# Optimization experiments

Hardware: AMD Instinct MI355X
Metric: run time of the kernel (lower is better)

Reference implementation:

```python
import jax, jax.numpy as jnp
import numpy as np

B, L, DM = 2, 1024, 768
DI = 2 * DM            # d_inner = 1536
NS = 16                # d_state
DTR = 48               # dt_rank
SCALE = 15             # scale_bits


def _dsp(x):
    # DampenedSquareplus: 0.5 * squareplus(x) = 0.25*(x + sqrt(x^2+4))
    return 0.25 * (x + jnp.sqrt(x * x + 4.0))


def _forward(hidden_states, gamma, W_in, b_in, conv_w, conv_b, W_x, b_x,
             W_dt, b_dt, W_out, b_out, base_decay_nums, res_gate, decay_shifts):
    residual = hidden_states
    # BitShiftNorm: center, then power-of-two RMS scale
    xm = hidden_states - hidden_states.mean(axis=-1, keepdims=True)
    var = (xm * xm).mean(axis=-1, keepdims=True)
    k = jnp.maximum(jnp.round(jnp.log2(jnp.sqrt(var + 1e-9))), 0.0)
    hs = xm * (2.0 ** (-k)) * gamma
    # in_proj (BitLinear modeled as linear)
    xz = hs @ W_in.T + b_in                      # [B,L,2*DI]
    x, z = jnp.split(xz, 2, axis=-1)             # each [B,L,DI]
    # causal depthwise conv1d (kernel 4, left pad 3, truncate to L)
    xt = jnp.transpose(x, (0, 2, 1))             # [B,DI,L]
    xt = jax.lax.conv_general_dilated(
        xt, conv_w, window_strides=(1,), padding=[(3, 0)],
        dimension_numbers=('NCH', 'OIH', 'NCH'), feature_group_count=DI)
    xt = xt + conv_b[None, :, None]
    x = jnp.transpose(xt, (0, 2, 1))             # [B,L,DI]
    x = _dsp(x)
    # x_proj -> dt, B_ssm, C_ssm
    x_dbl = x @ W_x.T + b_x                      # [B,L,DTR+2*NS]
    dt = x_dbl[..., :DTR]
    B_ssm = x_dbl[..., DTR:DTR + NS]
    C_ssm = x_dbl[..., DTR + NS:]
    decay_mod = dt @ W_dt.T + b_dt               # [B,L,DI]
    decay_nums = jnp.clip(base_decay_nums[None, None] + decay_mod[..., None], 0.0, 32767.0)  # [B,L,DI,NS]
    dt_val = _dsp(decay_mod) * 0.1               # [B,L,DI]
    u = (x * dt_val)[..., None] * B_ssm[:, :, None, :]   # [B,L,DI,NS]
    # dyadic decay: a = nums * 2^{-shift}
    a = decay_nums * (2.0 ** (-decay_shifts.astype(jnp.float32)))[None, None]
    F = DI * NS
    u_f = u.reshape(B, L, F)
    a_f = a.reshape(B, L, F)
    # linear recurrence h_t = a_t*h_{t-1} + u_t via associative scan over L
    def combine(c1, c2):
        a1, b1 = c1
        a2, b2 = c2
        return (a1 * a2, a2 * b1 + b2)
    _, h_f = jax.lax.associative_scan(combine, (a_f, u_f), axis=1)
    h_f = jnp.clip(h_f, -32000.0, 32000.0)
    h = h_f.reshape(B, L, DI, NS)
    y = jnp.einsum('bldn,bln->bld', h, C_ssm)    # [B,L,DI]
    # RationalSigmoid gate
    gate = 0.5 * (1.0 + z / jnp.sqrt(z * z + 1.0))
    y = y * gate
    out = y @ W_out.T + b_out
    out = jnp.clip(out, -32000.0, 32000.0)
    return residual + out * res_gate


def setup_inputs() -> dict:
    key = jax.random.key(0)
    ks = jax.random.split(key, 8)
    hidden_states = jax.random.normal(ks[0], (B, L, DM), jnp.float32)
    gamma = jnp.ones((DM,), jnp.float32)
    W_in = jax.random.normal(ks[1], (2 * DI, DM), jnp.float32) / np.float32(np.sqrt(DM))
    b_in = jnp.zeros((2 * DI,), jnp.float32)
    conv_w = jax.random.normal(ks[2], (DI, 1, 4), jnp.float32) * 0.5
    conv_b = jnp.zeros((DI,), jnp.float32)
    W_x = jax.random.normal(ks[3], (DTR + 2 * NS, DI), jnp.float32) / np.float32(np.sqrt(DI))
    b_x = jnp.zeros((DTR + 2 * NS,), jnp.float32)
    W_dt = jax.random.normal(ks[4], (DI, DTR), jnp.float32) * 0.001
    b_dt = jnp.zeros((DI,), jnp.float32)
    W_out = jax.random.normal(ks[5], (DM, DI), jnp.float32) * np.float32(0.02 / np.sqrt(24))
    b_out = jnp.zeros((DM,), jnp.float32)
    # HiPPO-S4D-real-like decays projected to dyadic with shift=15
    n = jnp.arange(NS, dtype=jnp.float32)
    decays = jnp.exp(-0.01 * (n + 1.0))
    base = jnp.round(decays * (2.0 ** SCALE))
    base_decay_nums = jnp.tile(base[None, :], (DI, 1))
    decay_shifts = jnp.full((DI, NS), SCALE, jnp.int32)
    res_gate = jnp.full((1,), 0.5, jnp.float32)  # nonzero so output depends on branch
    return dict(hidden_states=hidden_states, gamma=gamma, W_in=W_in, b_in=b_in,
                conv_w=conv_w, conv_b=conv_b, W_x=W_x, b_x=b_x, W_dt=W_dt, b_dt=b_dt,
                W_out=W_out, b_out=b_out, base_decay_nums=base_decay_nums,
                res_gate=res_gate, decay_shifts=decay_shifts)


def reference(hidden_states, gamma, W_in, b_in, conv_w, conv_b, W_x, b_x,
              W_dt, b_dt, W_out, b_out, base_decay_nums, res_gate, decay_shifts):
    return _forward(hidden_states, gamma, W_in, b_in, conv_w, conv_b, W_x, b_x,
                    W_dt, b_dt, W_out, b_out, base_decay_nums, res_gate, decay_shifts)
```

## Files before the change

kernel.cpp:

```cpp
#include <hip/hip_runtime.h>
#include <hip/hip_bf16.h>
#include <stdint.h>

#define BB  2
#define LL  1024
#define DMM 768
#define DII 1536
#define NSS 16
#define DTRR 48
#define XZN (2*DII)
#define NROWS (BB*LL)
#define N2 1664

#define CHUNKS 64
#define CHLEN  (LL/CHUNKS)
#define NCH    (BB*DII*NSS)

typedef _Float16 h16;
typedef __attribute__((ext_vector_type(8))) _Float16 h16x8;
typedef __attribute__((ext_vector_type(4))) float f32x4;

typedef const __attribute__((address_space(1))) uint32_t gau32;
typedef __attribute__((address_space(3))) uint32_t lau32;
#define GLL16(gp, lp) __builtin_amdgcn_global_load_lds((gau32*)(gp), (lau32*)(lp), 16, 0, 0)

__device__ __forceinline__ float dspf(float x) {
    return 0.25f * (x + sqrtf(x*x + 4.0f));
}
__device__ __forceinline__ float clampf(float x, float lo, float hi) {
    return fminf(fmaxf(x, lo), hi);
}

__global__ __launch_bounds__(256) void k_cvt(const float* __restrict__ in,
                                             h16* __restrict__ out, int n) {
    int i = blockIdx.x * 256 + threadIdx.x;
    if (i < n) out[i] = (h16)in[i];
}

__global__ __launch_bounds__(256) void k_w2(const float* __restrict__ W_x,
                                            const float* __restrict__ b_x,
                                            const float* __restrict__ W_dt,
                                            const float* __restrict__ b_dt,
                                            h16* __restrict__ W2,
                                            float* __restrict__ bias2) {
    int i = blockIdx.x;
    int tid = threadIdx.x;
    if (i < DII) {
        __shared__ float wd[DTRR];
        if (tid < DTRR) wd[tid] = W_dt[i * DTRR + tid];
        __syncthreads();
        for (int j = tid; j < DII; j += 256) {
            float s = 0.f;
            #pragma unroll
            for (int k = 0; k < DTRR; ++k) s = fmaf(wd[k], W_x[(size_t)k * DII + j], s);
            W2[(size_t)i * DII + j] = (h16)s;
        }
        if (tid == 0) {
            float s = b_dt[i];
            for (int k = 0; k < DTRR; ++k) s = fmaf(wd[k], b_x[k], s);
            bias2[i] = s;
        }
    } else if (i < DII + 2 * NSS) {
        int r = i - DII;
        for (int j = tid; j < DII; j += 256)
            W2[(size_t)i * DII + j] = (h16)W_x[(size_t)(DTRR + r) * DII + j];
        if (tid == 0) bias2[i] = b_x[DTRR + r];
    } else {
        for (int j = tid; j < DII; j += 256) W2[(size_t)i * DII + j] = (h16)0.f;
        if (tid == 0) bias2[i] = 0.f;
    }
}

__global__ __launch_bounds__(256) void k_norm(const float* __restrict__ hs,
                                              const float* __restrict__ gamma,
                                              h16* __restrict__ out) {
    int row = blockIdx.x;
    const float* p = hs + (size_t)row * DMM;
    __shared__ float red[256];
    int tid = threadIdx.x;

    float s = 0.f;
    for (int i = tid; i < DMM; i += 256) s += p[i];
    red[tid] = s; __syncthreads();
    for (int off = 128; off > 0; off >>= 1) {
        if (tid < off) red[tid] += red[tid + off];
        __syncthreads();
    }
    float mean = red[0] / (float)DMM;
    __syncthreads();

    float v = 0.f;
    for (int i = tid; i < DMM; i += 256) { float d = p[i] - mean; v += d*d; }
    red[tid] = v; __syncthreads();
    for (int off = 128; off > 0; off >>= 1) {
        if (tid < off) red[tid] += red[tid + off];
        __syncthreads();
    }
    float var = red[0] / (float)DMM;
    float k = rintf(log2f(sqrtf(var + 1e-9f)));
    k = fmaxf(k, 0.f);
    float scale = exp2f(-k);
    for (int i = tid; i < DMM; i += 256)
        out[(size_t)row * DMM + i] = (h16)((p[i] - mean) * scale * gamma[i]);
}

template<int EPI, typename OutT>
__global__ __launch_bounds__(256) void k_gemm64(
    const h16* __restrict__ A, int lda,
    const h16* __restrict__ Bw, int ldb,
    const float* __restrict__ bias,
    OutT* __restrict__ C, int ldc, int K,
    const float* __restrict__ resid, const float* __restrict__ rgate)
{
    __shared__ __align__(16) h16 As[2][64 * 64];
    __shared__ __align__(16) h16 Bs[2][64 * 64];
    const int tid  = threadIdx.x;
    const int lane = tid & 63;
    const int wv   = tid >> 6;

    const int nwg = gridDim.x * gridDim.y;
    const int bid = blockIdx.y * gridDim.x + blockIdx.x;
    const int cpx = nwg >> 3;
    const int swz = (bid & 7) * cpx + (bid >> 3);
    const int bxi = swz % gridDim.x, byi = swz / gridDim.x;

    const int bm = byi * 64, bn = bxi * 64;
    const int wr = wv >> 1, wc = wv & 1;

    f32x4 acc[2][2] = {};

    const int srow = lane >> 3;
    const int kbl  = ((lane & 7) ^ srow) * 8;
    const int KT = K / 64;

    #pragma unroll
    for (int q = 0; q < 2; ++q) {
        int row = (wv * 2 + q) * 8 + srow;
        GLL16(A  + (size_t)(bm + row) * lda + kbl, &As[0][(wv*2+q)*8*64]);
        GLL16(Bw + (size_t)(bn + row) * ldb + kbl, &Bs[0][(wv*2+q)*8*64]);
    }

    int buf = 0;
    for (int kt = 0; kt < KT; ++kt) {
        if (kt + 1 < KT) {
            int k0 = (kt + 1) * 64;
            #pragma unroll
            for (int q = 0; q < 2; ++q) {
                int row = (wv * 2 + q) * 8 + srow;
                GLL16(A  + (size_t)(bm + row) * lda + k0 + kbl, &As[buf^1][(wv*2+q)*8*64]);
                GLL16(Bw + (size_t)(bn + row) * ldb + k0 + kbl, &Bs[buf^1][(wv*2+q)*8*64]);
            }
            asm volatile("s_waitcnt vmcnt(4)" ::: "memory");
        } else {
            asm volatile("s_waitcnt vmcnt(0)" ::: "memory");
        }
        __syncthreads();

        const int r16 = lane & 15, kq = lane >> 4;
        #pragma unroll
        for (int kk = 0; kk < 2; ++kk) {
            h16x8 af[2], bf[2];
            #pragma unroll
            for (int i = 0; i < 2; ++i) {
                int rowA = wr * 32 + i * 16 + r16;
                af[i] = *(const h16x8*)&As[buf][rowA * 64 + (((kk*4 + kq) ^ (rowA & 7)) << 3)];
            }
            #pragma unroll
            for (int j = 0; j < 2; ++j) {
                int rowB = wc * 32 + j * 16 + r16;
                bf[j] = *(const h16x8*)&Bs[buf][rowB * 64 + (((kk*4 + kq) ^ (rowB & 7)) << 3)];
            }
            #pragma unroll
            for (int i = 0; i < 2; ++i)
                #pragma unroll
                for (int j = 0; j < 2; ++j)
                    acc[i][j] = __builtin_amdgcn_mfma_f32_16x16x32_f16(af[i], bf[j], acc[i][j], 0, 0, 0);
        }
        __syncthreads();
        buf ^= 1;
    }

    const int r4 = (lane >> 4) * 4;
    const int cn = lane & 15;
    float rg = 0.f;
    if (EPI) rg = rgate[0];
    #pragma unroll
    for (int i = 0; i < 2; ++i) {
        #pragma unroll
        for (int j = 0; j < 2; ++j) {
            int col = bn + wc * 32 + j * 16 + cn;
            float bv = bias[col];
            #pragma unroll
            for (int r = 0; r < 4; ++r) {
                int row = bm + wr * 32 + i * 16 + r4 + r;
                float v = acc[i][j][r] + bv;
                if (EPI) {
                    v = clampf(v, -32000.f, 32000.f);
                    v = resid[(size_t)row * ldc + col] + v * rg;
                }
                C[(size_t)row * ldc + col] = (OutT)v;
            }
        }
    }
}

__global__ __launch_bounds__(256) void k_conv(const h16* __restrict__ xz,
                                              const float* __restrict__ cw,
                                              const float* __restrict__ cb,
                                              h16* __restrict__ xacth)
{
    int idx = blockIdx.x * 256 + threadIdx.x;
    if (idx >= NROWS * DII) return;
    int c = idx % DII;
    int bl = idx / DII;
    int l = bl % LL;
    int b = bl / LL;
    float acc = cb[c];
    #pragma unroll
    for (int j = 0; j < 4; ++j) {
        int ls = l - 3 + j;
        if (ls >= 0)
            acc = fmaf((float)xz[(size_t)(b * LL + ls) * XZN + c], cw[c * 4 + j], acc);
    }
    xacth[idx] = (h16)dspf(acc);
}

__device__ __forceinline__ void load_setup(const float* __restrict__ basenum,
                                           const int* __restrict__ shifts,
                                           int d, float* base, float* p2c) {
    const float4* bp = (const float4*)(basenum + (size_t)d * NSS);
    const int4*   sp = (const int4*)(shifts + (size_t)d * NSS);
    #pragma unroll
    for (int q = 0; q < 4; ++q) {
        float4 bv = bp[q]; int4 sv = sp[q];
        base[q*4+0] = bv.x; base[q*4+1] = bv.y; base[q*4+2] = bv.z; base[q*4+3] = bv.w;
        p2c[q*4+0] = exp2f(-(float)sv.x);
        p2c[q*4+1] = exp2f(-(float)sv.y);
        p2c[q*4+2] = exp2f(-(float)sv.z);
        p2c[q*4+3] = exp2f(-(float)sv.w);
    }
}

__global__ __launch_bounds__(256) void k_scan_p1(
    const h16* __restrict__ dmbc,
    const h16* __restrict__ xacth,
    const float* __restrict__ basenum,
    const int*   __restrict__ shifts,
    float* __restrict__ stA, float* __restrict__ stH)
{
    int bc   = blockIdx.x / 6;
    int dblk = blockIdx.x % 6;
    int d    = dblk * 256 + threadIdx.x;
    int b    = bc / CHUNKS;
    int chunk= bc % CHUNKS;

    float base[16], p2c[16], h[16], A[16];
    load_setup(basenum, shifts, d, base, p2c);
    #pragma unroll
    for (int n = 0; n < 16; ++n) { h[n] = 0.f; A[n] = 1.f; }

    int row0 = b * LL + chunk * CHLEN;
    #pragma unroll 4
    for (int l = 0; l < CHLEN; ++l) {
        int row = row0 + l;
        float dm = (float)dmbc[(size_t)row * N2 + d];
        float xv = (float)xacth[(size_t)row * DII + d];
        float common = xv * (dspf(dm) * 0.1f);
        const h16x8* Bp = (const h16x8*)(dmbc + (size_t)row * N2 + DII);
        h16x8 b0 = Bp[0], b1 = Bp[1];
        float Bv[16];
        #pragma unroll
        for (int n = 0; n < 8; ++n) { Bv[n] = (float)b0[n]; Bv[8+n] = (float)b1[n]; }
        #pragma unroll
        for (int n = 0; n < 16; ++n) {
            float a = clampf(base[n] + dm, 0.f, 32767.f) * p2c[n];
            h[n] = fmaf(a, h[n], common * Bv[n]);
            A[n] *= a;
        }
    }
    size_t sb = ((size_t)bc * DII + d) * 16;
    float4* pa = (float4*)(stA + sb);
    float4* ph = (float4*)(stH + sb);
    #pragma unroll
    for (int q = 0; q < 4; ++q) {
        pa[q] = make_float4(A[q*4+0], A[q*4+1], A[q*4+2], A[q*4+3]);
        ph[q] = make_float4(h[q*4+0], h[q*4+1], h[q*4+2], h[q*4+3]);
    }
}

__global__ __launch_bounds__(256) void k_scan_p2(float* __restrict__ stA,
                                                 const float* __restrict__ stH)
{
    int ch = blockIdx.x * 256 + threadIdx.x;
    int b  = ch / (DII * NSS);
    int rem = ch - b * (DII * NSS);
    float hin = 0.f;
    #pragma unroll 4
    for (int c = 0; c < CHUNKS; ++c) {
        size_t idx = ((size_t)(b * CHUNKS + c) * (DII * NSS)) + rem;
        float a = stA[idx], hh = stH[idx];
        stA[idx] = hin;
        hin = fmaf(a, hin, hh);
    }
}

__global__ __launch_bounds__(256) void k_scan_p3(
    const h16* __restrict__ dmbc,
    const h16* __restrict__ xacth,
    const h16* __restrict__ xz,
    const float* __restrict__ basenum,
    const int*   __restrict__ shifts,
    const float* __restrict__ stA,
    h16* __restrict__ ygh)
{
    int bc   = blockIdx.x / 6;
    int dblk = blockIdx.x % 6;
    int d    = dblk * 256 + threadIdx.x;
    int b    = bc / CHUNKS;
    int chunk= bc % CHUNKS;

    float base[16], p2c[16], h[16];
    load_setup(basenum, shifts, d, base, p2c);
    size_t sb = ((size_t)bc * DII + d) * 16;
    const float4* pa = (const float4*)(stA + sb);
    #pragma unroll
    for (int q = 0; q < 4; ++q) {
        float4 v = pa[q];
        h[q*4+0] = v.x; h[q*4+1] = v.y; h[q*4+2] = v.z; h[q*4+3] = v.w;
    }

    int row0 = b * LL + chunk * CHLEN;
    #pragma unroll 4
    for (int l = 0; l < CHLEN; ++l) {
        int row = row0 + l;
        float dm = (float)dmbc[(size_t)row * N2 + d];
        float xv = (float)xacth[(size_t)row * DII + d];
        float common = xv * (dspf(dm) * 0.1f);
        const h16x8* Bp = (const h16x8*)(dmbc + (size_t)row * N2 + DII);
        h16x8 b0 = Bp[0], b1 = Bp[1], c0 = Bp[2], c1 = Bp[3];
        float Bv[16], Cv[16];
        #pragma unroll
        for (int n = 0; n < 8; ++n) {
            Bv[n] = (float)b0[n]; Bv[8+n] = (float)b1[n];
            Cv[n] = (float)c0[n]; Cv[8+n] = (float)c1[n];
        }
        float y = 0.f;
        #pragma unroll
        for (int n = 0; n < 16; ++n) {
            float a = clampf(base[n] + dm, 0.f, 32767.f) * p2c[n];
            h[n] = fmaf(a, h[n], common * Bv[n]);
            float hc = clampf(h[n], -32000.f, 32000.f);
            y = fmaf(hc, Cv[n], y);
        }
        float z = (float)xz[(size_t)row * XZN + DII + d];
        float gate = 0.5f * (1.0f + z * rsqrtf(z * z + 1.0f));
        ygh[(size_t)row * DII + d] = (h16)(y * gate);
    }
}

extern "C" void kernel_launch(void* const* d_in, const int* in_sizes, int n_in,
                              void* d_out, int out_size, void* d_ws, size_t ws_size,
                              hipStream_t stream) {
    const float* hs        = (const float*)d_in[0];
    const float* gamma     = (const float*)d_in[1];
    const float* W_in      = (const float*)d_in[2];
    const float* b_in      = (const float*)d_in[3];
    const float* conv_w    = (const float*)d_in[4];
    const float* conv_b    = (const float*)d_in[5];
    const float* W_x       = (const float*)d_in[6];
    const float* b_x       = (const float*)d_in[7];
    const float* W_dt      = (const float*)d_in[8];
    const float* b_dt      = (const float*)d_in[9];
    const float* W_out     = (const float*)d_in[10];
    const float* b_out     = (const float*)d_in[11];
    const float* base_dec  = (const float*)d_in[12];
    const float* res_gate  = (const float*)d_in[13];
    const int*   dec_shift = (const int*)d_in[14];

    char* w = (char*)d_ws;
    h16*   XZH   = (h16*)w;    w += (size_t)NROWS * XZN * 2;
    h16*   XACTH = (h16*)w;    w += (size_t)NROWS * DII * 2;
    h16*   DMBCH = (h16*)w;    w += (size_t)NROWS * N2  * 2;
    h16*   W2H   = (h16*)w;    w += (size_t)N2 * DII * 2;
    h16*   WOH   = (h16*)w;    w += (size_t)DMM * DII * 2;
    float* BIAS2 = (float*)w;  w += 8192;
    h16*   YGH   = (h16*)w;    w += (size_t)NROWS * DII * 2;
    h16*   HSNH  = (h16*)w;    w += (size_t)NROWS * DMM * 2;
    h16*   WINH  = (h16*)w;    w += (size_t)XZN * DMM * 2;
    float* STA   = (float*)w;  w += (size_t)BB * CHUNKS * DII * NSS * 4;
    float* STH   = (float*)w;  w += (size_t)BB * CHUNKS * DII * NSS * 4;

    float* out = (float*)d_out;

    k_cvt<<<(XZN * DMM + 255) / 256, 256, 0, stream>>>(W_in, WINH, XZN * DMM);
    k_cvt<<<(DMM * DII + 255) / 256, 256, 0, stream>>>(W_out, WOH, DMM * DII);
    k_w2<<<N2, 256, 0, stream>>>(W_x, b_x, W_dt, b_dt, W2H, BIAS2);

    k_norm<<<NROWS, 256, 0, stream>>>(hs, gamma, HSNH);

    k_gemm64<0, h16><<<dim3(XZN / 64, NROWS / 64), 256, 0, stream>>>(
        HSNH, DMM, WINH, DMM, b_in, XZH, XZN, DMM, nullptr, nullptr);

    k_conv<<<(NROWS * DII) / 256, 256, 0, stream>>>(XZH, conv_w, conv_b, XACTH);

    k_gemm64<0, h16><<<dim3(N2 / 64, NROWS / 64), 256, 0, stream>>>(
        XACTH, DII, W2H, DII, BIAS2, DMBCH, N2, DII, nullptr, nullptr);

    k_scan_p1<<<BB * CHUNKS * 6, 256, 0, stream>>>(
        DMBCH, XACTH, base_dec, dec_shift, STA, STH);
    k_scan_p2<<<NCH / 256, 256, 0, stream>>>(STA, STH);
    k_scan_p3<<<BB * CHUNKS * 6, 256, 0, stream>>>(
        DMBCH, XACTH, XZH, base_dec, dec_shift, STA, YGH);

    k_gemm64<1, float><<<dim3(DMM / 64, NROWS / 64), 256, 0, stream>>>(
        YGH, DII, WOH, DII, b_out, out, DMM, DII, hs, res_gate);
}
```

Baseline: 176.6 us.

## Load GEMM B-operand directly to registers and vectorize norm, conv, conversion kernels

The GEMM now stages only A through LDS and loads B fragments straight from global memory into registers with a manually unrolled two-stage ping-pong, and its tile-index swizzle is changed to column-major block order. The z-gate activation moves into the in_proj GEMM epilogue, removing that work from the scan kernel. Norm uses one wave per row with float4 loads and shuffle reductions, conv processes 8 channels per thread with vector loads, and the two weight-conversion kernels merge into one launch. The direct B loads skip LDS reuse across waves, so B traffic rises and the load latency may be exposed.

After: 239.7 us. 1.36x slower.

```diff
diff --git a/kernel.cpp b/kernel.cpp
--- a/kernel.cpp
+++ b/kernel.cpp
@@ -31,10 +31,13 @@
     return fminf(fmaxf(x, lo), hi);
 }
 
-__global__ __launch_bounds__(256) void k_cvt(const float* __restrict__ in,
-                                             h16* __restrict__ out, int n) {
+__global__ __launch_bounds__(256) void k_cvt2(const float* __restrict__ in1,
+                                              h16* __restrict__ out1, int n1,
+                                              const float* __restrict__ in2,
+                                              h16* __restrict__ out2, int n2) {
     int i = blockIdx.x * 256 + threadIdx.x;
-    if (i < n) out[i] = (h16)in[i];
+    if (i < n1) out1[i] = (h16)in1[i];
+    else if (i < n1 + n2) out2[i - n1] = (h16)in2[i - n1];
 }
 
 __global__ __launch_bounds__(256) void k_w2(const float* __restrict__ W_x,
@@ -74,38 +77,43 @@
 __global__ __launch_bounds__(256) void k_norm(const float* __restrict__ hs,
                                               const float* __restrict__ gamma,
                                               h16* __restrict__ out) {
-    int row = blockIdx.x;
+    int row  = blockIdx.x * 4 + (threadIdx.x >> 6);
+    int lane = threadIdx.x & 63;
     const float* p = hs + (size_t)row * DMM;
-    __shared__ float red[256];
-    int tid = threadIdx.x;
-
-    float s = 0.f;
-    for (int i = tid; i < DMM; i += 256) s += p[i];
-    red[tid] = s; __syncthreads();
-    for (int off = 128; off > 0; off >>= 1) {
-        if (tid < off) red[tid] += red[tid + off];
-        __syncthreads();
-    }
-    float mean = red[0] / (float)DMM;
-    __syncthreads();
-
-    float v = 0.f;
-    for (int i = tid; i < DMM; i += 256) { float d = p[i] - mean; v += d*d; }
-    red[tid] = v; __syncthreads();
-    for (int off = 128; off > 0; off >>= 1) {
-        if (tid < off) red[tid] += red[tid + off];
-        __syncthreads();
-    }
-    float var = red[0] / (float)DMM;
+    float4 v0 = *(const float4*)&p[lane * 4];
+    float4 v1 = *(const float4*)&p[256 + lane * 4];
+    float4 v2 = *(const float4*)&p[512 + lane * 4];
+    float s = v0.x+v0.y+v0.z+v0.w + v1.x+v1.y+v1.z+v1.w + v2.x+v2.y+v2.z+v2.w;
+    #pragma unroll
+    for (int off = 32; off > 0; off >>= 1) s += __shfl_xor(s, off);
+    float mean = s * (1.0f / (float)DMM);
+    float vv = 0.f;
+    #pragma unroll
+    for (int q = 0; q < 4; ++q) {
+        float d0 = ((const float*)&v0)[q] - mean; vv += d0*d0;
+        float d1 = ((const float*)&v1)[q] - mean; vv += d1*d1;
+        float d2 = ((const float*)&v2)[q] - mean; vv += d2*d2;
+    }
+    #pragma unroll
+    for (int off = 32; off > 0; off >>= 1) vv += __shfl_xor(vv, off);
+    float var = vv * (1.0f / (float)DMM);
     float k = rintf(log2f(sqrtf(var + 1e-9f)));
     k = fmaxf(k, 0.f);
     float scale = exp2f(-k);
-    for (int i = tid; i < DMM; i += 256)
-        out[(size_t)row * DMM + i] = (h16)((p[i] - mean) * scale * gamma[i]);
+    float4 g0 = *(const float4*)&gamma[lane * 4];
+    float4 g1 = *(const float4*)&gamma[256 + lane * 4];
+    float4 g2 = *(const float4*)&gamma[512 + lane * 4];
+    h16* o = out + (size_t)row * DMM;
+    #pragma unroll
+    for (int q = 0; q < 4; ++q) {
+        o[lane*4 + q]       = (h16)((((const float*)&v0)[q] - mean) * scale * ((const float*)&g0)[q]);
+        o[256 + lane*4 + q] = (h16)((((const float*)&v1)[q] - mean) * scale * ((const float*)&g1)[q]);
+        o[512 + lane*4 + q] = (h16)((((const float*)&v2)[q] - mean) * scale * ((const float*)&g2)[q]);
+    }
 }
 
 template<int EPI, typename OutT>
-__global__ __launch_bounds__(256) void k_gemm64(
+__global__ __launch_bounds__(256) void k_gemm_bd(
     const h16* __restrict__ A, int lda,
     const h16* __restrict__ Bw, int ldb,
     const float* __restrict__ bias,
@@ -113,17 +121,16 @@
     const float* __restrict__ resid, const float* __restrict__ rgate)
 {
     __shared__ __align__(16) h16 As[2][64 * 64];
-    __shared__ __align__(16) h16 Bs[2][64 * 64];
     const int tid  = threadIdx.x;
     const int lane = tid & 63;
     const int wv   = tid >> 6;
 
-    const int nwg = gridDim.x * gridDim.y;
-    const int bid = blockIdx.y * gridDim.x + blockIdx.x;
+    const int gy = gridDim.y;
+    const int nwg = gridDim.x * gy;
+    const int bid0 = blockIdx.x * gy + blockIdx.y;
     const int cpx = nwg >> 3;
-    const int swz = (bid & 7) * cpx + (bid >> 3);
-    const int bxi = swz % gridDim.x, byi = swz / gridDim.x;
-
+    const int swz = (bid0 & 7) * cpx + (bid0 >> 3);
+    const int bxi = swz / gy, byi = swz % gy;
     const int bm = byi * 64, bn = bxi * 64;
     const int wr = wv >> 1, wc = wv & 1;
 
@@ -133,57 +140,71 @@
     const int kbl  = ((lane & 7) ^ srow) * 8;
     const int KT = K / 64;
 
-    #pragma unroll
-    for (int q = 0; q < 2; ++q) {
-        int row = (wv * 2 + q) * 8 + srow;
-        GLL16(A  + (size_t)(bm + row) * lda + kbl, &As[0][(wv*2+q)*8*64]);
-        GLL16(Bw + (size_t)(bn + row) * ldb + kbl, &Bs[0][(wv*2+q)*8*64]);
-    }
-
-    int buf = 0;
-    for (int kt = 0; kt < KT; ++kt) {
-        if (kt + 1 < KT) {
-            int k0 = (kt + 1) * 64;
-            #pragma unroll
-            for (int q = 0; q < 2; ++q) {
-                int row = (wv * 2 + q) * 8 + srow;
-                GLL16(A  + (size_t)(bm + row) * lda + k0 + kbl, &As[buf^1][(wv*2+q)*8*64]);
-                GLL16(Bw + (size_t)(bn + row) * ldb + k0 + kbl, &Bs[buf^1][(wv*2+q)*8*64]);
-            }
-            asm volatile("s_waitcnt vmcnt(4)" ::: "memory");
+    const int r16 = lane & 15, kq = lane >> 4;
+    const size_t bofs0 = (size_t)(bn + wc * 32 + r16) * ldb + (kq << 3);
+    const size_t bofs1 = bofs0 + (size_t)16 * ldb;
+
+    h16x8 bfA[2][2], bfB[2][2];
+
+#define STAGEA(dstbuf, k0) do { \
+    _Pragma("unroll") \
+    for (int q = 0; q < 2; ++q) { \
+        int row_ = (wv * 2 + q) * 8 + srow; \
+        GLL16(A + (size_t)(bm + row_) * lda + (k0) + kbl, &As[dstbuf][(wv*2+q)*8*64]); \
+    } } while (0)
+
+#define LOADB(BF, k0) do { \
+    BF[0][0] = *(const h16x8*)&Bw[bofs0 + (k0)]; \
+    BF[0][1] = *(const h16x8*)&Bw[bofs1 + (k0)]; \
+    BF[1][0] = *(const h16x8*)&Bw[bofs0 + (k0) + 32]; \
+    BF[1][1] = *(const h16x8*)&Bw[bofs1 + (k0) + 32]; \
+    } while (0)
+
+#define COMPUTE(abuf, BF) do { \
+    _Pragma("unroll") \
+    for (int kk = 0; kk < 2; ++kk) { \
+        int rowA0 = wr * 32 + r16, rowA1 = rowA0 + 16; \
+        h16x8 af0 = *(const h16x8*)&As[abuf][rowA0 * 64 + (((kk*4 + kq) ^ (rowA0 & 7)) << 3)]; \
+        h16x8 af1 = *(const h16x8*)&As[abuf][rowA1 * 64 + (((kk*4 + kq) ^ (rowA1 & 7)) << 3)]; \
+        acc[0][0] = __builtin_amdgcn_mfma_f32_16x16x32_f16(af0, BF[kk][0], acc[0][0], 0, 0, 0); \
+        acc[0][1] = __builtin_amdgcn_mfma_f32_16x16x32_f16(af0, BF[kk][1], acc[0][1], 0, 0, 0); \
+        acc[1][0] = __builtin_amdgcn_mfma_f32_16x16x32_f16(af1, BF[kk][0], acc[1][0], 0, 0, 0); \
+        acc[1][1] = __builtin_amdgcn_mfma_f32_16x16x32_f16(af1, BF[kk][1], acc[1][1], 0, 0, 0); \
+    } } while (0)
+
+    STAGEA(0, 0);
+    LOADB(bfA, 0);
+
+    for (int ktp = 0; ktp < KT; ktp += 2) {
+        if (ktp + 1 < KT) {
+            STAGEA(1, (ktp + 1) * 64);
+            LOADB(bfB, (ktp + 1) * 64);
+            asm volatile("s_waitcnt vmcnt(6)" ::: "memory");
         } else {
             asm volatile("s_waitcnt vmcnt(0)" ::: "memory");
         }
         __syncthreads();
-
-        const int r16 = lane & 15, kq = lane >> 4;
-        #pragma unroll
-        for (int kk = 0; kk < 2; ++kk) {
-            h16x8 af[2], bf[2];
-            #pragma unroll
-            for (int i = 0; i < 2; ++i) {
-                int rowA = wr * 32 + i * 16 + r16;
-                af[i] = *(const h16x8*)&As[buf][rowA * 64 + (((kk*4 + kq) ^ (rowA & 7)) << 3)];
-            }
-            #pragma unroll
-            for (int j = 0; j < 2; ++j) {
-                int rowB = wc * 32 + j * 16 + r16;
-                bf[j] = *(const h16x8*)&Bs[buf][rowB * 64 + (((kk*4 + kq) ^ (rowB & 7)) << 3)];
-            }
-            #pragma unroll
-            for (int i = 0; i < 2; ++i)
-                #pragma unroll
-                for (int j = 0; j < 2; ++j)
-                    acc[i][j] = __builtin_amdgcn_mfma_f32_16x16x32_f16(af[i], bf[j], acc[i][j], 0, 0, 0);
-        }
+        COMPUTE(0, bfA);
         __syncthreads();
-        buf ^= 1;
-    }
+        if (ktp + 2 < KT) {
+            STAGEA(0, (ktp + 2) * 64);
+            LOADB(bfA, (ktp + 2) * 64);
+            asm volatile("s_waitcnt vmcnt(6)" ::: "memory");
+        } else {
+            asm volatile("s_waitcnt vmcnt(0)" ::: "memory");
+        }
+        __syncthreads();
+        COMPUTE(1, bfB);
+        __syncthreads();
+    }
+#undef STAGEA
+#undef LOADB
+#undef COMPUTE
 
     const int r4 = (lane >> 4) * 4;
     const int cn = lane & 15;
     float rg = 0.f;
-    if (EPI) rg = rgate[0];
+    if (EPI == 1) rg = rgate[0];
     #pragma unroll
     for (int i = 0; i < 2; ++i) {
         #pragma unroll
@@ -194,9 +215,12 @@
             for (int r = 0; r < 4; ++r) {
                 int row = bm + wr * 32 + i * 16 + r4 + r;
                 float v = acc[i][j][r] + bv;
-                if (EPI) {
+                if (EPI == 1) {
                     v = clampf(v, -32000.f, 32000.f);
                     v = resid[(size_t)row * ldc + col] + v * rg;
+                }
+                if (EPI == 2) {
+                    if (col >= DII) v = 0.5f * (1.0f + v * rsqrtf(v * v + 1.0f));
                 }
                 C[(size_t)row * ldc + col] = (OutT)v;
             }
@@ -210,19 +234,34 @@
                                               h16* __restrict__ xacth)
 {
     int idx = blockIdx.x * 256 + threadIdx.x;
-    if (idx >= NROWS * DII) return;
-    int c = idx % DII;
-    int bl = idx / DII;
+    if (idx >= NROWS * (DII / 8)) return;
+    int c8 = idx % (DII / 8);
+    int bl = idx / (DII / 8);
     int l = bl % LL;
     int b = bl / LL;
-    float acc = cb[c];
-    #pragma unroll
-    for (int j = 0; j < 4; ++j) {
-        int ls = l - 3 + j;
-        if (ls >= 0)
-            acc = fmaf((float)xz[(size_t)(b * LL + ls) * XZN + c], cw[c * 4 + j], acc);
-    }
-    xacth[idx] = (h16)dspf(acc);
+    int c0 = c8 * 8;
+
+    float acc[8];
+    float4 wv[8];
+    #pragma unroll
+    for (int j = 0; j < 8; ++j) {
+        acc[j] = cb[c0 + j];
+        wv[j] = *(const float4*)&cw[(c0 + j) * 4];
+    }
+    #pragma unroll
+    for (int t = 0; t < 4; ++t) {
+        int ls = l - 3 + t;
+        if (ls >= 0) {
+            h16x8 xv = *(const h16x8*)&xz[(size_t)(b * LL + ls) * XZN + c0];
+            #pragma unroll
+            for (int j = 0; j < 8; ++j)
+                acc[j] = fmaf((float)xv[j], ((const float*)&wv[j])[t], acc[j]);
+        }
+    }
+    h16x8 o;
+    #pragma unroll
+    for (int j = 0; j < 8; ++j) o[j] = (h16)dspf(acc[j]);
+    *(h16x8*)&xacth[(size_t)bl * DII + c0] = o;
 }
 
 __device__ __forceinline__ void load_setup(const float* __restrict__ basenum,
@@ -352,8 +391,7 @@
             float hc = clampf(h[n], -32000.f, 32000.f);
             y = fmaf(hc, Cv[n], y);
         }
-        float z = (float)xz[(size_t)row * XZN + DII + d];
-        float gate = 0.5f * (1.0f + z * rsqrtf(z * z + 1.0f));
+        float gate = (float)xz[(size_t)row * XZN + DII + d];
         ygh[(size_t)row * DII + d] = (h16)(y * gate);
     }
 }
@@ -392,18 +430,18 @@
 
     float* out = (float*)d_out;
 
-    k_cvt<<<(XZN * DMM + 255) / 256, 256, 0, stream>>>(W_in, WINH, XZN * DMM);
-    k_cvt<<<(DMM * DII + 255) / 256, 256, 0, stream>>>(W_out, WOH, DMM * DII);
+    k_cvt2<<<(XZN * DMM + DMM * DII + 255) / 256, 256, 0, stream>>>(
+        W_in, WINH, XZN * DMM, W_out, WOH, DMM * DII);
     k_w2<<<N2, 256, 0, stream>>>(W_x, b_x, W_dt, b_dt, W2H, BIAS2);
 
-    k_norm<<<NROWS, 256, 0, stream>>>(hs, gamma, HSNH);
-
-    k_gemm64<0, h16><<<dim3(XZN / 64, NROWS / 64), 256, 0, stream>>>(
+    k_norm<<<NROWS / 4, 256, 0, stream>>>(hs, gamma, HSNH);
+
+    k_gemm_bd<2, h16><<<dim3(XZN / 64, NROWS / 64), 256, 0, stream>>>(
         HSNH, DMM, WINH, DMM, b_in, XZH, XZN, DMM, nullptr, nullptr);
 
-    k_conv<<<(NROWS * DII) / 256, 256, 0, stream>>>(XZH, conv_w, conv_b, XACTH);
-
-    k_gemm64<0, h16><<<dim3(N2 / 64, NROWS / 64), 256, 0, stream>>>(
+    k_conv<<<(NROWS * (DII / 8)) / 256, 256, 0, stream>>>(XZH, conv_w, conv_b, XACTH);
+
+    k_gemm_bd<0, h16><<<dim3(N2 / 64, NROWS / 64), 256, 0, stream>>>(
         XACTH, DII, W2H, DII, BIAS2, DMBCH, N2, DII, nullptr, nullptr);
 
     k_scan_p1<<<BB * CHUNKS * 6, 256, 0, stream>>>(
@@ -412,6 +450,6 @@
     k_scan_p3<<<BB * CHUNKS * 6, 256, 0, stream>>>(
         DMBCH, XACTH, XZH, base_dec, dec_shift, STA, YGH);
 
-    k_gemm64<1, float><<<dim3(DMM / 64, NROWS / 64), 256, 0, stream>>>(
+    k_gemm_bd<1, float><<<dim3(DMM / 64, NROWS / 64), 256, 0, stream>>>(
         YGH, DII, WOH, DII, b_out, out, DMM, DII, hs, res_gate);
 }
```
